# Performance work log

Hardware: AMD Instinct MI355X
Metric: run time of the kernel (lower is better)

## Reference

```python
import jax, jax.numpy as jnp
import numpy as np

N, E, B = 10000, 160000, 64
ND, ED, H, L, C = 128, 64, 256, 4, 10
LN_EPS = 1e-5


def _layernorm(x, g, b):
    mu = jnp.mean(x, axis=-1, keepdims=True)
    var = jnp.mean(jnp.square(x - mu), axis=-1, keepdims=True)
    return (x - mu) * jax.lax.rsqrt(var + LN_EPS) * g + b


def setup_inputs() -> dict:
    key = jax.random.key(0)
    ks = jax.random.split(key, 24)

    def w(k, shape, fan_in):
        return jax.random.normal(k, shape, jnp.float32) * (1.0 / np.sqrt(fan_in))

    node_features = jax.random.normal(ks[0], (N, ND), jnp.float32)
    edge_index = jax.random.randint(ks[1], (2, E), 0, N, jnp.int64)
    edge_features = jax.random.normal(ks[2], (E, ED), jnp.float32)
    # deterministic sorted batch assignment (no empty graphs)
    batch = (jnp.arange(N, dtype=jnp.int64) * B) // N

    inp = dict(
        node_features=node_features,
        edge_index=edge_index,
        edge_features=edge_features,
        batch=batch,
        node_W=w(ks[3], (ND, H), ND), node_b=jnp.zeros((H,), jnp.float32),
        edge_W=w(ks[4], (ED, H), ED), edge_b=jnp.zeros((H,), jnp.float32),
        msg_W1=w(ks[5], (L, 3 * H, H), 3 * H), msg_b1=jnp.zeros((L, H), jnp.float32),
        msg_W2=w(ks[6], (L, H, H), H), msg_b2=jnp.zeros((L, H), jnp.float32),
        upd_W1=w(ks[7], (L, 2 * H, H), 2 * H), upd_b1=jnp.zeros((L, H), jnp.float32),
        upd_W2=w(ks[8], (L, H, H), H), upd_b2=jnp.zeros((L, H), jnp.float32),
        ln_g=jnp.ones((L, H), jnp.float32), ln_b=jnp.zeros((L, H), jnp.float32),
        ro_W1=w(ks[9], (H, H), H), ro_b1=jnp.zeros((H,), jnp.float32),
        ro_W2=w(ks[10], (H, C), H), ro_b2=jnp.zeros((C,), jnp.float32),
    )
    return inp


def _forward(node_features, edge_features, node_W, node_b, edge_W, edge_b,
             msg_W1, msg_b1, msg_W2, msg_b2, upd_W1, upd_b1, upd_W2, upd_b2,
             ln_g, ln_b, ro_W1, ro_b1, ro_W2, ro_b2, edge_index, batch):
    src, dst = edge_index[0], edge_index[1]
    x = node_features @ node_W + node_b            # [N, H]
    edge_attr = edge_features @ edge_W + edge_b    # [E, H]
    for l in range(L):
        # batched gather-MLP over all edges (vectorized version of the per-edge loop)
        m_in = jnp.concatenate([x[src], x[dst], edge_attr], axis=-1)  # [E, 3H]
        msg = jax.nn.relu(m_in @ msg_W1[l] + msg_b1[l]) @ msg_W2[l] + msg_b2[l]
        agg = jnp.zeros_like(x).at[dst].add(msg)    # scatter-add by destination
        u_in = jnp.concatenate([x, agg], axis=-1)   # [N, 2H]
        upd = jax.nn.relu(u_in @ upd_W1[l] + upd_b1[l]) @ upd_W2[l] + upd_b2[l]
        x = _layernorm(x + upd, ln_g[l], ln_b[l])
    # global mean pool per graph
    sums = jax.ops.segment_sum(x, batch, num_segments=B)
    cnts = jax.ops.segment_sum(jnp.ones((x.shape[0], 1), x.dtype), batch, num_segments=B)
    pooled = sums / cnts                            # [B, H]
    return jax.nn.relu(pooled @ ro_W1 + ro_b1) @ ro_W2 + ro_b2  # [B, C]


def reference(node_features, edge_index, edge_features, batch,
              node_W, node_b, edge_W, edge_b,
              msg_W1, msg_b1, msg_W2, msg_b2,
              upd_W1, upd_b1, upd_W2, upd_b2,
              ln_g, ln_b, ro_W1, ro_b1, ro_W2, ro_b2):
    return _forward(node_features, edge_features, node_W, node_b, edge_W, edge_b,
                    msg_W1, msg_b1, msg_W2, msg_b2, upd_W1, upd_b1, upd_W2, upd_b2,
                    ln_g, ln_b, ro_W1, ro_b1, ro_W2, ro_b2, edge_index, batch)
```

## Files before the change

### kernel.cpp

```cpp
#include <hip/hip_runtime.h>
#include <cstdint>
#include <cstddef>


typedef unsigned short u16;
typedef __attribute__((ext_vector_type(4))) float f32x4;
typedef __attribute__((ext_vector_type(8))) short bf16x8;
typedef __attribute__((ext_vector_type(4))) short s16x4;

constexpr int kN  = 10000;
constexpr int kE  = 160000;
constexpr int kB  = 64;
constexpr int kH  = 256;
constexpr int kL  = 4;
constexpr int kC  = 10;
constexpr float kEps = 1e-5f;

struct __align__(16) F4 { float v[4]; };
__device__ __forceinline__ F4 ldF4(const float* p) { return *reinterpret_cast<const F4*>(p); }

__device__ __forceinline__ u16 f2bf(float f) {
    unsigned u = __builtin_bit_cast(unsigned, f);
    return (u16)((u + 0x7fffu + ((u >> 16) & 1u)) >> 16);
}
__device__ __forceinline__ float bf2f(u16 h) {
    return __builtin_bit_cast(float, (unsigned)h << 16);
}
__device__ __forceinline__ unsigned cvtpk(float lo, float hi) {
    unsigned r;
    asm("v_cvt_pk_bf16_f32 %0, %1, %2" : "=v"(r) : "v"(lo), "v"(hi));
    return r;
}

typedef __attribute__((address_space(1))) void GV;
typedef __attribute__((address_space(3))) void LV;
__device__ __forceinline__ void gl_lds16(const void* g, void* l) {
    __builtin_amdgcn_global_load_lds((GV*)g, (LV*)l, 16, 0, 0);
}
__device__ __forceinline__ void dma_w16k(const u16* __restrict__ Wc, char* lds, int tid) {
    const int w = tid >> 6, lane = tid & 63;
    char* lb = lds + w * 4096;
    const char* gb = (const char*)Wc + w * 4096 + lane * 16;
    #pragma unroll
    for (int i = 0; i < 4; ++i) gl_lds16(gb + i * 1024, lb + i * 1024);
}

__global__ void k_detect_i64(const unsigned* __restrict__ w, int* __restrict__ flag) {
    if (threadIdx.x == 0 && blockIdx.x == 0) {
        int is64 = 1;
        for (int i = 0; i < 64; ++i)
            if (w[2*i + 1] != 0u) { is64 = 0; break; }
        *flag = is64;
    }
}
__global__ void k_cvt_idx(const unsigned* __restrict__ w, const int* __restrict__ flag,
                          int* __restrict__ out, int n) {
    int i = blockIdx.x * 256 + threadIdx.x;
    if (i < n) out[i] = (*flag) ? (int)w[2*i] : (int)w[i];
}

__global__ __launch_bounds__(256) void k_hist(const int* __restrict__ dst,
                                              int* __restrict__ cnt) {
    int e = blockIdx.x * 256 + threadIdx.x;
    if (e < kE) atomicAdd(&cnt[dst[e]], 1);
}
__global__ __launch_bounds__(256) void k_scan(const int* __restrict__ cnt,
                                              int* __restrict__ cur) {
    __shared__ int part[256];
    const int t = threadIdx.x;
    const int per = (kN + 255) / 256;
    int s = 0;
    for (int i = 0; i < per; ++i) {
        int idx = t * per + i;
        if (idx < kN) s += cnt[idx];
    }
    int own = s;
    part[t] = s; __syncthreads();
    for (int off = 1; off < 256; off <<= 1) {
        int v = (t >= off) ? part[t - off] : 0;
        __syncthreads();
        part[t] += v;
        __syncthreads();
    }
    int run = part[t] - own;
    for (int i = 0; i < per; ++i) {
        int idx = t * per + i;
        if (idx < kN) { cur[idx] = run; run += cnt[idx]; }
    }
}
__global__ __launch_bounds__(256) void k_scatter(
    const int* __restrict__ src, const int* __restrict__ dst,
    int* __restrict__ cur, int* __restrict__ perm,
    int* __restrict__ ssorted, int* __restrict__ dsorted) {
    int e = blockIdx.x * 256 + threadIdx.x;
    if (e < kE) {
        int d = dst[e];
        int p = atomicAdd(&cur[d], 1);
        perm[p] = e;
        ssorted[p] = src[e];
        dsorted[p] = d;
    }
}

__global__ __launch_bounds__(256) void k_prep_w(
    const float* __restrict__ mW1, const float* __restrict__ mW2,
    const float* __restrict__ uW1, const float* __restrict__ uW2,
    u16* __restrict__ tm1, u16* __restrict__ tm2,
    u16* __restrict__ tu1, u16* __restrict__ tu2)
{
    int idx = blockIdx.x * 256 + threadIdx.x;
    const int S1 = kL * 768 * 256;
    const int S2 = S1 + kL * 256 * 256;
    const int S3 = S2 + kL * 512 * 256;
    const int S4 = S3 + kL * 256 * 256;
    const float* src; u16* dst; int K, r;
    if (idx < S1)      { src = mW1; dst = tm1; K = 768; r = idx; }
    else if (idx < S2) { src = mW2; dst = tm2; K = 256; r = idx - S1; }
    else if (idx < S3) { src = uW1; dst = tu1; K = 512; r = idx - S2; }
    else if (idx < S4) { src = uW2; dst = tu2; K = 256; r = idx - S3; }
    else return;
    int per = K * 256;
    int layer = r / per, rr = r - layer * per;
    int k = rr >> 8, n = rr & 255;
    int kc = k >> 5, kg = (k >> 3) & 3, e = k & 7;
    dst[(size_t)layer * per + (size_t)kc * 8192 + n * 32 + ((kg ^ ((n >> 1) & 3)) << 3) + e]
        = f2bf(src[(size_t)layer * per + rr]);
}

__global__ __launch_bounds__(256) void k_prep_ef(
    const float* __restrict__ ef, const int* __restrict__ perm,
    u16* __restrict__ efs)
{
    int idx = blockIdx.x * 256 + threadIdx.x;
    if (idx >= kE * 64) return;
    int p = idx >> 6, k = idx & 63;
    float v = ef[(size_t)perm[p] * 64 + k];
    int row = p & 63, blk = p >> 6;
    int kc = k >> 5, kg = (k >> 3) & 3, e = k & 7;
    efs[(size_t)blk * 4096 + kc * 2048 + row * 32
        + ((kg ^ ((row >> 1) & 3)) << 3) + e] = f2bf(v);
}

__global__ __launch_bounds__(256) void k_prep_m(
    const float* __restrict__ eW, const float* __restrict__ eb,
    const float* __restrict__ mW1, const float* __restrict__ mb1,
    u16* __restrict__ tmc, float* __restrict__ b1p)
{
    __shared__ float sWe[16 * 256];
    const int l = blockIdx.x, rq = blockIdx.y, t = threadIdx.x;
    const int r0 = rq * 16;
    #pragma unroll
    for (int i = 0; i < 16; ++i) sWe[i * 256 + t] = eW[(size_t)(r0 + i) * 256 + t];
    __syncthreads();
    const float* W1c = mW1 + (size_t)l * 768 * 256 + (size_t)512 * 256;
    float m[16];
    #pragma unroll
    for (int r = 0; r < 16; ++r) m[r] = 0.f;
    float bp = (rq == 0) ? mb1[l * 256 + t] : 0.f;
    for (int j = 0; j < 256; ++j) {
        float wv = W1c[(size_t)j * 256 + t];
        if (rq == 0) bp = fmaf(eb[j], wv, bp);
        #pragma unroll
        for (int r = 0; r < 16; ++r) m[r] = fmaf(sWe[r * 256 + j], wv, m[r]);
    }
    if (rq == 0) b1p[l * 256 + t] = bp;
    #pragma unroll
    for (int r = 0; r < 16; ++r) {
        int k = r0 + r;
        int kc = k >> 5, kg = (k >> 3) & 3, e = k & 7;
        tmc[(size_t)l * 16384 + (size_t)kc * 8192 + t * 32
            + ((kg ^ ((t >> 1) & 3)) << 3) + e] = f2bf(m[r]);
    }
}

__global__ __launch_bounds__(256) void k_encode_nodes(
    const float* __restrict__ nf, const float* __restrict__ W,
    const float* __restrict__ b, float* __restrict__ x, u16* __restrict__ x_bf)
{
    __shared__ float s_nf[4 * 128];
    const int n0 = blockIdx.x * 4;
    const int tid = threadIdx.x;
    reinterpret_cast<float2*>(s_nf)[tid] =
        reinterpret_cast<const float2*>(nf + (size_t)n0 * 128)[tid];
    __syncthreads();
    float acc[4] = {0.f, 0.f, 0.f, 0.f};
    for (int k = 0; k < 128; ++k) {
        float w = W[k * kH + tid];
        #pragma unroll
        for (int r = 0; r < 4; ++r) acc[r] = fmaf(s_nf[r * 128 + k], w, acc[r]);
    }
    float bias = b[tid];
    #pragma unroll
    for (int r = 0; r < 4; ++r) {
        float o = acc[r] + bias;
        x[(size_t)(n0 + r) * kH + tid] = o;
        x_bf[(size_t)(n0 + r) * kH + tid] = f2bf(o);
    }
}

__device__ __forceinline__ bf16x8 rdfrag(const char* lds, int n, int kg) {
    return *reinterpret_cast<const bf16x8*>(lds + n * 64 + ((kg ^ ((n >> 1) & 3)) << 4));
}
__device__ __forceinline__ bf16x8 rdH(const char* H, int row, int kbyte) {
    return *reinterpret_cast<const bf16x8*>(H + row * 512 + (kbyte ^ ((row & 7) << 4)));
}

__global__ __launch_bounds__(256, 3) void k_node_pre(
    const u16* __restrict__ x_bf, const u16* __restrict__ Wt1,
    u16* __restrict__ y_a, u16* __restrict__ y_b)
{
    __shared__ char sWt[16384];
    __shared__ char sA[4096];
    const int tid = threadIdx.x;
    const int n0 = blockIdx.x * 64;
    const int half = blockIdx.y;
    const u16* Wt = Wt1 + (size_t)half * 8 * 8192;
    u16* y = half ? y_b : y_a;
    const int w = tid >> 6, lane = tid & 63;
    const int lr = lane & 15, lg = lane >> 4;
    const int srow = tid >> 2, skg = tid & 3;
    const int kg_src = skg ^ ((srow >> 1) & 3);
    int gnode = n0 + srow; if (gnode >= kN) gnode = kN - 1;

    f32x4 acc[4][4];
    #pragma unroll
    for (int i = 0; i < 4; ++i)
        #pragma unroll
        for (int j = 0; j < 4; ++j) acc[i][j] = (f32x4){0.f, 0.f, 0.f, 0.f};

    for (int kc = 0; kc < 8; ++kc) {
        __syncthreads();
        dma_w16k(Wt + (size_t)kc * 8192, sWt, tid);
        gl_lds16(x_bf + (size_t)gnode * kH + kc * 32 + kg_src * 8, sA + w * 1024);
        __syncthreads();
        bf16x8 af[4], bfm[4];
        #pragma unroll
        for (int i = 0; i < 4; ++i) af[i] = rdfrag(sWt, w * 64 + i * 16 + lr, lg);
        #pragma unroll
        for (int j = 0; j < 4; ++j) bfm[j] = rdfrag(sA, j * 16 + lr, lg);
        #pragma unroll
        for (int i = 0; i < 4; ++i)
            #pragma unroll
            for (int j = 0; j < 4; ++j)
                acc[i][j] = __builtin_amdgcn_mfma_f32_16x16x32_bf16(af[i], bfm[j], acc[i][j], 0, 0, 0);
    }
    #pragma unroll
    for (int i = 0; i < 4; ++i) {
        const int hc0 = w * 64 + i * 16 + lg * 4;
        #pragma unroll
        for (int j = 0; j < 4; ++j) {
            const int node = n0 + j * 16 + lr;
            if (node < kN) {
                uint2 o;
                o.x = cvtpk(acc[i][j][0], acc[i][j][1]);
                o.y = cvtpk(acc[i][j][2], acc[i][j][3]);
                *reinterpret_cast<uint2*>(y + (size_t)node * kH + hc0) = o;
            }
        }
    }
}

__global__ __launch_bounds__(256, 3) void k_msg(
    const u16* __restrict__ efs,
    const int* __restrict__ ssorted, const int* __restrict__ dsorted,
    const u16* __restrict__ y_a, const u16* __restrict__ y_b,
    const u16* __restrict__ Wtm, const float* __restrict__ b1p,
    const u16* __restrict__ Wt2, const float* __restrict__ b2,
    float* __restrict__ agg)
{
    __shared__ char sWt[16384];
    __shared__ char sA[4096];
    __shared__ char sH[32768];
    __shared__ int sDst[64];

    const int tid = threadIdx.x;
    const int nwg = gridDim.x;
    const int q8 = nwg >> 3, r8 = nwg & 7;
    const int xcd = blockIdx.x & 7, sub = blockIdx.x >> 3;
    const int bid = (xcd < r8 ? xcd * (q8 + 1) : r8 * (q8 + 1) + (xcd - r8) * q8) + sub;
    const int e0 = bid * 64;

    const int w = tid >> 6, lane = tid & 63;
    const int lr = lane & 15, lg = lane >> 4;

    if (tid < 64) sDst[tid] = dsorted[e0 + tid];
    int esrc[4], edst[4];
    #pragma unroll
    for (int j = 0; j < 4; ++j) {
        esrc[j] = ssorted[e0 + j * 16 + lr];
        edst[j] = dsorted[e0 + j * 16 + lr];
    }

    f32x4 acc[4][4];
    #pragma unroll
    for (int i = 0; i < 4; ++i)
        #pragma unroll
        for (int j = 0; j < 4; ++j) acc[i][j] = (f32x4){0.f, 0.f, 0.f, 0.f};

    for (int kc = 0; kc < 2; ++kc) {
        __syncthreads();
        dma_w16k(Wtm + (size_t)kc * 8192, sWt, tid);
        gl_lds16((const char*)efs + (size_t)bid * 8192 + kc * 4096 + w * 1024 + lane * 16,
                 sA + w * 1024);
        __syncthreads();
        bf16x8 af[4], bfm[4];
        #pragma unroll
        for (int i = 0; i < 4; ++i) af[i] = rdfrag(sWt, w * 64 + i * 16 + lr, lg);
        #pragma unroll
        for (int j = 0; j < 4; ++j) bfm[j] = rdfrag(sA, j * 16 + lr, lg);
        #pragma unroll
        for (int i = 0; i < 4; ++i)
            #pragma unroll
            for (int j = 0; j < 4; ++j)
                acc[i][j] = __builtin_amdgcn_mfma_f32_16x16x32_bf16(af[i], bfm[j], acc[i][j], 0, 0, 0);
    }

    #pragma unroll
    for (int j = 0; j < 4; ++j) {
        const int edge = j * 16 + lr;
        const u16* pa = y_a + (size_t)esrc[j] * kH;
        const u16* pb = y_b + (size_t)edst[j] * kH;
        uint2 ya[4], yb[4];
        #pragma unroll
        for (int i = 0; i < 4; ++i) {
            const int hc0 = w * 64 + i * 16 + lg * 4;
            ya[i] = *reinterpret_cast<const uint2*>(pa + hc0);
            yb[i] = *reinterpret_cast<const uint2*>(pb + hc0);
        }
        #pragma unroll
        for (int i = 0; i < 4; ++i) {
            const int hc0 = w * 64 + i * 16 + lg * 4;
            const F4 bb = ldF4(b1p + hc0);
            float s0 = __builtin_bit_cast(float, ya[i].x << 16) + __builtin_bit_cast(float, yb[i].x << 16);
            float s1 = __builtin_bit_cast(float, ya[i].x & 0xffff0000u) + __builtin_bit_cast(float, yb[i].x & 0xffff0000u);
            float s2 = __builtin_bit_cast(float, ya[i].y << 16) + __builtin_bit_cast(float, yb[i].y << 16);
            float s3 = __builtin_bit_cast(float, ya[i].y & 0xffff0000u) + __builtin_bit_cast(float, yb[i].y & 0xffff0000u);
            float h0 = acc[i][j][0] + bb.v[0] + s0; h0 = h0 > 0.f ? h0 : 0.f;
            float h1 = acc[i][j][1] + bb.v[1] + s1; h1 = h1 > 0.f ? h1 : 0.f;
            float h2 = acc[i][j][2] + bb.v[2] + s2; h2 = h2 > 0.f ? h2 : 0.f;
            float h3 = acc[i][j][3] + bb.v[3] + s3; h3 = h3 > 0.f ? h3 : 0.f;
            uint2 o; o.x = cvtpk(h0, h1); o.y = cvtpk(h2, h3);
            int byte = edge * 512 + hc0 * 2;
            *reinterpret_cast<uint2*>(sH + (byte ^ ((edge & 7) << 4))) = o;
            acc[i][j] = (f32x4){0.f, 0.f, 0.f, 0.f};
        }
    }
    __syncthreads();

    for (int kc = 0; kc < 8; ++kc) {
        __syncthreads();
        dma_w16k(Wt2 + (size_t)kc * 8192, sWt, tid);
        __syncthreads();
        bf16x8 af2[4], bf2[4];
        #pragma unroll
        for (int i = 0; i < 4; ++i) af2[i] = rdH(sH, i * 16 + lr, kc * 64 + lg * 16);
        #pragma unroll
        for (int j = 0; j < 4; ++j) bf2[j] = rdfrag(sWt, w * 64 + j * 16 + lr, lg);
        #pragma unroll
        for (int i = 0; i < 4; ++i)
            #pragma unroll
            for (int j = 0; j < 4; ++j)
                acc[i][j] = __builtin_amdgcn_mfma_f32_16x16x32_bf16(af2[i], bf2[j], acc[i][j], 0, 0, 0);
    }

    __syncthreads();
    #pragma unroll
    for (int j = 0; j < 4; ++j) {
        const int oc = w * 64 + j * 16 + lr;
        const float b2v = b2[oc];
        #pragma unroll
        for (int i = 0; i < 4; ++i) {
            unsigned p01 = cvtpk(acc[i][j][0] + b2v, acc[i][j][1] + b2v);
            unsigned p23 = cvtpk(acc[i][j][2] + b2v, acc[i][j][3] + b2v);
            int eb0 = i * 16 + lg * 4;
            *reinterpret_cast<u16*>(sH + (((eb0 + 0) * 512 + oc * 2) ^ (((eb0 + 0) & 7) << 4))) = (u16)p01;
            *reinterpret_cast<u16*>(sH + (((eb0 + 1) * 512 + oc * 2) ^ (((eb0 + 1) & 7) << 4))) = (u16)(p01 >> 16);
            *reinterpret_cast<u16*>(sH + (((eb0 + 2) * 512 + oc * 2) ^ (((eb0 + 2) & 7) << 4))) = (u16)p23;
            *reinterpret_cast<u16*>(sH + (((eb0 + 3) * 512 + oc * 2) ^ (((eb0 + 3) & 7) << 4))) = (u16)(p23 >> 16);
        }
    }
    __syncthreads();

    {
        const int col = tid;
        float run = 0.f;
        int prev = sDst[0];
        #pragma unroll 1
        for (int eb = 0; eb < 8; ++eb) {
            float vv[8]; int dd[8];
            #pragma unroll
            for (int t = 0; t < 8; ++t) {
                int e = eb * 8 + t;
                int byte = e * 512 + col * 2;
                vv[t] = bf2f(*reinterpret_cast<const u16*>(sH + (byte ^ ((e & 7) << 4))));
                dd[t] = sDst[e];
            }
            #pragma unroll
            for (int t = 0; t < 8; ++t) {
                if (dd[t] != prev) {
                    unsafeAtomicAdd(agg + (size_t)prev * kH + col, run);
                    run = 0.f; prev = dd[t];
                }
                run += vv[t];
            }
        }
        unsafeAtomicAdd(agg + (size_t)prev * kH + col, run);
    }
}

__global__ __launch_bounds__(256, 2) void k_upd(
    float* __restrict__ x, u16* __restrict__ x_bf,
    float* __restrict__ agg,
    const u16* __restrict__ Wt1, const float* __restrict__ b1,
    const u16* __restrict__ Wt2, const float* __restrict__ b2,
    const float* __restrict__ lng, const float* __restrict__ lnb,
    const u16* __restrict__ Wt1n, int do_y,
    u16* __restrict__ y_a, u16* __restrict__ y_b)
{
    __shared__ char sWt[2][16384];
    __shared__ char sA[2][4096];
    __shared__ char sH[32768];

    const int tid = threadIdx.x;
    const int n0 = blockIdx.x * 64;
    const int w = tid >> 6, lane = tid & 63;
    const int lr = lane & 15, lg = lane >> 4;
    const int srow = tid >> 2, skg = tid & 3;
    const int kg_src = skg ^ ((srow >> 1) & 3);
    int gnode = n0 + srow; if (gnode >= kN) gnode = kN - 1;

    dma_w16k(Wt1, sWt[0], tid);
    gl_lds16(x_bf + (size_t)gnode * kH + kg_src * 8, sA[0] + w * 1024);

    f32x4 acc[4][4];
    #pragma unroll
    for (int i = 0; i < 4; ++i)
        #pragma unroll
        for (int j = 0; j < 4; ++j) acc[i][j] = (f32x4){0.f, 0.f, 0.f, 0.f};
    __syncthreads();

    for (int kc = 0; kc < 16; ++kc) {
        const int cur = kc & 1, nxt = cur ^ 1;
        bool do_agg = false; F4 a0, a1;
        if (kc < 15) {
            dma_w16k(Wt1 + (size_t)(kc + 1) * 8192, sWt[nxt], tid);
            if (kc + 1 < 8) {
                gl_lds16(x_bf + (size_t)gnode * kH + (kc + 1) * 32 + kg_src * 8,
                         sA[nxt] + w * 1024);
            } else {
                const float* ap = agg + (size_t)gnode * kH + (kc + 1 - 8) * 32 + skg * 8;
                a0 = ldF4(ap); a1 = ldF4(ap + 4); do_agg = true;
            }
        } else {
            dma_w16k(Wt2, sWt[nxt], tid);
        }
        bf16x8 af[4], bfm[4];
        #pragma unroll
        for (int i = 0; i < 4; ++i) af[i] = rdfrag(sWt[cur], w * 64 + i * 16 + lr, lg);
        #pragma unroll
        for (int j = 0; j < 4; ++j) bfm[j] = rdfrag(sA[cur], j * 16 + lr, lg);
        #pragma unroll
        for (int i = 0; i < 4; ++i)
            #pragma unroll
            for (int j = 0; j < 4; ++j)
                acc[i][j] = __builtin_amdgcn_mfma_f32_16x16x32_bf16(af[i], bfm[j], acc[i][j], 0, 0, 0);
        if (do_agg) {
            int4 bv;
            bv.x = (int)cvtpk(a0.v[0], a0.v[1]);
            bv.y = (int)cvtpk(a0.v[2], a0.v[3]);
            bv.z = (int)cvtpk(a1.v[0], a1.v[1]);
            bv.w = (int)cvtpk(a1.v[2], a1.v[3]);
            *reinterpret_cast<int4*>(sA[nxt] + srow * 64 + ((skg ^ ((srow >> 1) & 3)) << 4)) = bv;
        }
        __syncthreads();
    }

    #pragma unroll
    for (int i = 0; i < 4; ++i) {
        const int hc0 = w * 64 + i * 16 + lg * 4;
        const F4 bb = ldF4(b1 + hc0);
        #pragma unroll
        for (int j = 0; j < 4; ++j) {
            const int row = j * 16 + lr;
            float h0 = acc[i][j][0] + bb.v[0]; h0 = h0 > 0.f ? h0 : 0.f;
            float h1 = acc[i][j][1] + bb.v[1]; h1 = h1 > 0.f ? h1 : 0.f;
            float h2 = acc[i][j][2] + bb.v[2]; h2 = h2 > 0.f ? h2 : 0.f;
            float h3 = acc[i][j][3] + bb.v[3]; h3 = h3 > 0.f ? h3 : 0.f;
            uint2 o; o.x = cvtpk(h0, h1); o.y = cvtpk(h2, h3);
            int byte = row * 512 + hc0 * 2;
            *reinterpret_cast<uint2*>(sH + (byte ^ ((row & 7) << 4))) = o;
            acc[i][j] = (f32x4){0.f, 0.f, 0.f, 0.f};
        }
    }
    __syncthreads();

    {
        float4 z = make_float4(0.f, 0.f, 0.f, 0.f);
        float4* bp = reinterpret_cast<float4*>(agg + (size_t)n0 * kH);
        #pragma unroll
        for (int i = 0; i < 16; ++i) {
            int idx = i * 256 + tid;
            int row = idx >> 6;
            if (n0 + row < kN) bp[idx] = z;
        }
    }

    for (int kc = 0; kc < 8; ++kc) {
        const int cur = kc & 1, nxt = cur ^ 1;
        if (kc < 7) dma_w16k(Wt2 + (size_t)(kc + 1) * 8192, sWt[nxt], tid);
        bf16x8 af2[4], bf2[4];
        #pragma unroll
        for (int i = 0; i < 4; ++i) af2[i] = rdH(sH, i * 16 + lr, kc * 64 + lg * 16);
        #pragma unroll
        for (int j = 0; j < 4; ++j) bf2[j] = rdfrag(sWt[cur], w * 64 + j * 16 + lr, lg);
        #pragma unroll
        for (int i = 0; i < 4; ++i)
            #pragma unroll
            for (int j = 0; j < 4; ++j)
                acc[i][j] = __builtin_amdgcn_mfma_f32_16x16x32_bf16(af2[i], bf2[j], acc[i][j], 0, 0, 0);
        __syncthreads();
    }

    float b2v[4], gv[4], bvn[4];
    #pragma unroll
    for (int j = 0; j < 4; ++j) {
        int oc = w * 64 + j * 16 + lr;
        b2v[j] = b2[oc]; gv[j] = lng[oc]; bvn[j] = lnb[oc];
    }
    #pragma unroll
    for (int i = 0; i < 4; ++i)
        #pragma unroll
        for (int j = 0; j < 4; ++j) {
            int oc = w * 64 + j * 16 + lr;
            #pragma unroll
            for (int q = 0; q < 4; ++q) {
                int node = n0 + i * 16 + lg * 4 + q;
                int ncl = node < kN ? node : kN - 1;
                acc[i][j][q] += b2v[j] + x[(size_t)ncl * kH + oc];
            }
        }

    float (*red)[64][2] = reinterpret_cast<float(*)[64][2]>(sA[0]);
    float2* mstd = reinterpret_cast<float2*>(sA[0] + 2048);
    __syncthreads();
    #pragma unroll
    for (int i = 0; i < 4; ++i)
        #pragma unroll
        for (int q = 0; q < 4; ++q) {
            float s = acc[i][0][q] + acc[i][1][q] + acc[i][2][q] + acc[i][3][q];
            float ss = acc[i][0][q] * acc[i][0][q] + acc[i][1][q] * acc[i][1][q]
                     + acc[i][2][q] * acc[i][2][q] + acc[i][3][q] * acc[i][3][q];
            #pragma unroll
            for (int m = 1; m < 16; m <<= 1) { s += __shfl_xor(s, m); ss += __shfl_xor(ss, m); }
            if (lr == 0) { red[w][i * 16 + lg * 4 + q][0] = s; red[w][i * 16 + lg * 4 + q][1] = ss; }
        }
    __syncthreads();
    if (tid < 64) {
        float s = red[0][tid][0] + red[1][tid][0] + red[2][tid][0] + red[3][tid][0];
        float ss = red[0][tid][1] + red[1][tid][1] + red[2][tid][1] + red[3][tid][1];
        float mean = s * (1.f / 256.f);
        float var = ss * (1.f / 256.f) - mean * mean;
        mstd[tid] = make_float2(mean, rsqrtf(var + kEps));
    }
    __syncthreads();
    #pragma unroll
    for (int i = 0; i < 4; ++i)
        #pragma unroll
        for (int j = 0; j < 4; ++j) {
            int oc = w * 64 + j * 16 + lr;
            #pragma unroll
            for (int q = 0; q < 4; ++q) {
                int nn = i * 16 + lg * 4 + q;
                int node = n0 + nn;
                if (node < kN) {
                    float2 ms = mstd[nn];
                    float o = (acc[i][j][q] - ms.x) * ms.y * gv[j] + bvn[j];
                    u16 ob = f2bf(o);
                    x[(size_t)node * kH + oc] = o;
                    x_bf[(size_t)node * kH + oc] = ob;
                    if (do_y) {
                        int byte = nn * 512 + oc * 2;
                        *reinterpret_cast<u16*>(sH + (byte ^ ((nn & 7) << 4))) = ob;
                    }
                }
            }
        }

    if (do_y) {
        __syncthreads();
        dma_w16k(Wt1n, sWt[0], tid);
        #pragma unroll
        for (int i = 0; i < 4; ++i)
            #pragma unroll
            for (int j = 0; j < 4; ++j) acc[i][j] = (f32x4){0.f, 0.f, 0.f, 0.f};
        __syncthreads();
        for (int c = 0; c < 16; ++c) {
            const int cur = c & 1;
            if (c < 15) dma_w16k(Wt1n + (size_t)(c + 1) * 8192, sWt[cur ^ 1], tid);
            bf16x8 af[4], bfm[4];
            #pragma unroll
            for (int i = 0; i < 4; ++i) af[i] = rdfrag(sWt[cur], w * 64 + i * 16 + lr, lg);
            #pragma unroll
            for (int j = 0; j < 4; ++j) bfm[j] = rdH(sH, j * 16 + lr, (c & 7) * 64 + lg * 16);
            #pragma unroll
            for (int i = 0; i < 4; ++i)
                #pragma unroll
                for (int j = 0; j < 4; ++j)
                    acc[i][j] = __builtin_amdgcn_mfma_f32_16x16x32_bf16(af[i], bfm[j], acc[i][j], 0, 0, 0);
            if (c == 7 || c == 15) {
                u16* y = (c == 7) ? y_a : y_b;
                #pragma unroll
                for (int i = 0; i < 4; ++i) {
                    const int hc0 = w * 64 + i * 16 + lg * 4;
                    #pragma unroll
                    for (int j = 0; j < 4; ++j) {
                        const int node = n0 + j * 16 + lr;
                        if (node < kN) {
                            uint2 o;
                            o.x = cvtpk(acc[i][j][0], acc[i][j][1]);
                            o.y = cvtpk(acc[i][j][2], acc[i][j][3]);
                            *reinterpret_cast<uint2*>(y + (size_t)node * kH + hc0) = o;
                        }
                        acc[i][j] = (f32x4){0.f, 0.f, 0.f, 0.f};
                    }
                }
            }
            __syncthreads();
        }
    }
}

__device__ __forceinline__ int lower_bound_i(const int* a, int n, int v) {
    int lo = 0, hi = n;
    while (lo < hi) { int m = (lo + hi) >> 1; if (a[m] < v) lo = m + 1; else hi = m; }
    return lo;
}

__global__ __launch_bounds__(256) void k_pool_ro(
    const float* __restrict__ x, const int* __restrict__ batch,
    const float* __restrict__ W1, const float* __restrict__ b1,
    const float* __restrict__ W2, const float* __restrict__ b2,
    float* __restrict__ out)
{
    __shared__ float ph[kH];
    __shared__ float h1[kH];
    const int b = blockIdx.x, t = threadIdx.x;
    const int s = lower_bound_i(batch, kN, b);
    const int e = lower_bound_i(batch, kN, b + 1);
    float acc = 0.f;
    for (int i = s; i < e; ++i) acc += x[(size_t)i * kH + t];
    ph[t] = acc / (float)(e - s);
    __syncthreads();
    float a = b1[t];
    for (int k = 0; k < kH; ++k) a = fmaf(ph[k], W1[k * kH + t], a);
    h1[t] = a > 0.f ? a : 0.f;
    __syncthreads();
    if (t < kC) {
        float o = b2[t];
        for (int k = 0; k < kH; ++k) o = fmaf(h1[k], W2[k * kC + t], o);
        out[b * kC + t] = o;
    }
}

extern "C" void kernel_launch(void* const* d_in, const int* in_sizes, int n_in,
                              void* d_out, int out_size, void* d_ws, size_t ws_size,
                              hipStream_t stream)
{
    const float* nf     = (const float*)d_in[0];
    const void*  ei_raw = d_in[1];
    const float* ef     = (const float*)d_in[2];
    const void*  ba_raw = d_in[3];
    const float* node_W = (const float*)d_in[4];
    const float* node_b = (const float*)d_in[5];
    const float* edge_W = (const float*)d_in[6];
    const float* edge_b = (const float*)d_in[7];
    const float* msg_W1 = (const float*)d_in[8];
    const float* msg_b1 = (const float*)d_in[9];
    const float* msg_W2 = (const float*)d_in[10];
    const float* msg_b2 = (const float*)d_in[11];
    const float* upd_W1 = (const float*)d_in[12];
    const float* upd_b1 = (const float*)d_in[13];
    const float* upd_W2 = (const float*)d_in[14];
    const float* upd_b2 = (const float*)d_in[15];
    const float* ln_g   = (const float*)d_in[16];
    const float* ln_b   = (const float*)d_in[17];
    const float* ro_W1  = (const float*)d_in[18];
    const float* ro_b1  = (const float*)d_in[19];
    const float* ro_W2  = (const float*)d_in[20];
    const float* ro_b2  = (const float*)d_in[21];

    char* p = (char*)d_ws;
    auto alloc = [&](size_t bytes) { char* r = p; p += (bytes + 255) & ~(size_t)255; return r; };
    float* x    = (float*)alloc((size_t)kN * kH * 4);
    float* agg  = (float*)alloc((size_t)kN * kH * 4);
    u16* x_bf   = (u16*)alloc((size_t)kN * kH * 2);
    u16* y_a    = (u16*)alloc((size_t)kN * kH * 2);
    u16* y_b    = (u16*)alloc((size_t)kN * kH * 2);
    u16* efs    = (u16*)alloc((size_t)kE * 64 * 2);
    u16* tm1 = (u16*)alloc((size_t)kL * 768 * 256 * 2);
    u16* tm2 = (u16*)alloc((size_t)kL * 256 * 256 * 2);
    u16* tu1 = (u16*)alloc((size_t)kL * 512 * 256 * 2);
    u16* tu2 = (u16*)alloc((size_t)kL * 256 * 256 * 2);
    u16* tmc = (u16*)alloc((size_t)kL * 64 * 256 * 2);
    float* b1p = (float*)alloc((size_t)kL * 256 * 4);
    int* ei32 = (int*)alloc((size_t)2 * kE * 4);
    int* ba32 = (int*)alloc((size_t)kN * 4);
    int* cnt  = (int*)alloc((size_t)kN * 4);
    int* cur  = (int*)alloc((size_t)kN * 4);
    int* perm = (int*)alloc((size_t)kE * 4);
    int* ssorted = (int*)alloc((size_t)kE * 4);
    int* dsorted = (int*)alloc((size_t)kE * 4);
    int* flag = (int*)alloc(4);

    k_detect_i64<<<1, 64, 0, stream>>>((const unsigned*)ei_raw, flag);
    k_cvt_idx<<<(2 * kE + 255) / 256, 256, 0, stream>>>((const unsigned*)ei_raw, flag, ei32, 2 * kE);
    k_cvt_idx<<<(kN + 255) / 256, 256, 0, stream>>>((const unsigned*)ba_raw, flag, ba32, kN);
    const int* src = ei32;
    const int* dst = ei32 + kE;

    hipMemsetAsync(cnt, 0, (size_t)kN * 4, stream);
    k_hist<<<(kE + 255) / 256, 256, 0, stream>>>(dst, cnt);
    k_scan<<<1, 256, 0, stream>>>(cnt, cur);
    k_scatter<<<(kE + 255) / 256, 256, 0, stream>>>(src, dst, cur, perm, ssorted, dsorted);

    const int prep_elems = kL * (768 + 256 + 512 + 256) * 256;
    k_prep_w<<<(prep_elems + 255) / 256, 256, 0, stream>>>(
        msg_W1, msg_W2, upd_W1, upd_W2, tm1, tm2, tu1, tu2);
    k_prep_m<<<dim3(kL, 4), 256, 0, stream>>>(edge_W, edge_b, msg_W1, msg_b1, tmc, b1p);
    k_prep_ef<<<(kE * 64 + 255) / 256, 256, 0, stream>>>(ef, perm, efs);

    k_encode_nodes<<<kN / 4, 256, 0, stream>>>(nf, node_W, node_b, x, x_bf);

    hipMemsetAsync(agg, 0, (size_t)kN * kH * sizeof(float), stream);
    k_node_pre<<<dim3((kN + 63) / 64, 2), 256, 0, stream>>>(x_bf, tm1, y_a, y_b);

    for (int l = 0; l < kL; ++l) {
        k_msg<<<kE / 64, 256, 0, stream>>>(efs, ssorted, dsorted, y_a, y_b,
            tmc + (size_t)l * 64 * 256, b1p + l * 256,
            tm2 + (size_t)l * 256 * 256, msg_b2 + l * kH, agg);
        const int do_y = (l < kL - 1) ? 1 : 0;
        k_upd<<<(kN + 63) / 64, 256, 0, stream>>>(x, x_bf, agg,
            tu1 + (size_t)l * 512 * 256, upd_b1 + l * kH,
            tu2 + (size_t)l * 256 * 256, upd_b2 + l * kH,
            ln_g + l * kH, ln_b + l * kH,
            tm1 + (size_t)(l + 1 < kL ? l + 1 : 0) * 768 * 256, do_y, y_a, y_b);
    }

    k_pool_ro<<<kB, 256, 0, stream>>>(x, ba32, ro_W1, ro_b1, ro_W2, ro_b2, (float*)d_out);
}
```

Measured before the change: 658.6 us.

## Read msg weights from global directly, split node projection out of update kernel

k_msg no longer stages weight and edge-feature tiles in LDS with barriers. It reads MFMA fragments straight from global memory, prefetches the gathered y rows up front and raises the occupancy hint to 4. The next-layer node projection that was fused into k_upd moves back to a separate k_node_pre launch per layer, which adds an extra pass over x_bf per layer but simplifies k_upd. k_prep_ef now reads edge features coalesced and scatters writes via a rank array instead of gathering through perm. The risk is uncached, uncoalesced weight-fragment reads in k_msg and more register pressure from the prefetched y values.

After: 607.0 us. -7.8%, faster.

```diff
diff --git a/kernel.cpp b/kernel.cpp
--- a/kernel.cpp
+++ b/kernel.cpp
@@ -43,6 +43,16 @@
     const char* gb = (const char*)Wc + w * 4096 + lane * 16;
     #pragma unroll
     for (int i = 0; i < 4; ++i) gl_lds16(gb + i * 1024, lb + i * 1024);
+}
+
+__device__ __forceinline__ bf16x8 g_frag(const u16* __restrict__ g, int n, int kg) {
+    return *reinterpret_cast<const bf16x8*>(g + n * 32 + ((kg ^ ((n >> 1) & 3)) << 3));
+}
+__device__ __forceinline__ bf16x8 rdfrag(const char* lds, int n, int kg) {
+    return *reinterpret_cast<const bf16x8*>(lds + n * 64 + ((kg ^ ((n >> 1) & 3)) << 4));
+}
+__device__ __forceinline__ bf16x8 rdH(const char* H, int row, int kbyte) {
+    return *reinterpret_cast<const bf16x8*>(H + row * 512 + (kbyte ^ ((row & 7) << 4)));
 }
 
 __global__ void k_detect_i64(const unsigned* __restrict__ w, int* __restrict__ flag) {
@@ -90,13 +100,13 @@
 }
 __global__ __launch_bounds__(256) void k_scatter(
     const int* __restrict__ src, const int* __restrict__ dst,
-    int* __restrict__ cur, int* __restrict__ perm,
+    int* __restrict__ cur, int* __restrict__ rank,
     int* __restrict__ ssorted, int* __restrict__ dsorted) {
     int e = blockIdx.x * 256 + threadIdx.x;
     if (e < kE) {
         int d = dst[e];
         int p = atomicAdd(&cur[d], 1);
-        perm[p] = e;
+        rank[e] = p;
         ssorted[p] = src[e];
         dsorted[p] = d;
     }
@@ -128,17 +138,18 @@
 }
 
 __global__ __launch_bounds__(256) void k_prep_ef(
-    const float* __restrict__ ef, const int* __restrict__ perm,
+    const float* __restrict__ ef, const int* __restrict__ rank,
     u16* __restrict__ efs)
 {
     int idx = blockIdx.x * 256 + threadIdx.x;
     if (idx >= kE * 64) return;
-    int p = idx >> 6, k = idx & 63;
-    float v = ef[(size_t)perm[p] * 64 + k];
+    int e = idx >> 6, k = idx & 63;
+    float v = ef[idx];
+    int p = rank[e];
     int row = p & 63, blk = p >> 6;
-    int kc = k >> 5, kg = (k >> 3) & 3, e = k & 7;
+    int kc = k >> 5, kg = (k >> 3) & 3, ee = k & 7;
     efs[(size_t)blk * 4096 + kc * 2048 + row * 32
-        + ((kg ^ ((row >> 1) & 3)) << 3) + e] = f2bf(v);
+        + ((kg ^ ((row >> 1) & 3)) << 3) + ee] = f2bf(v);
 }
 
 __global__ __launch_bounds__(256) void k_prep_m(
@@ -196,13 +207,6 @@
         x[(size_t)(n0 + r) * kH + tid] = o;
         x_bf[(size_t)(n0 + r) * kH + tid] = f2bf(o);
     }
-}
-
-__device__ __forceinline__ bf16x8 rdfrag(const char* lds, int n, int kg) {
-    return *reinterpret_cast<const bf16x8*>(lds + n * 64 + ((kg ^ ((n >> 1) & 3)) << 4));
-}
-__device__ __forceinline__ bf16x8 rdH(const char* H, int row, int kbyte) {
-    return *reinterpret_cast<const bf16x8*>(H + row * 512 + (kbyte ^ ((row & 7) << 4)));
 }
 
 __global__ __launch_bounds__(256, 3) void k_node_pre(
@@ -260,7 +264,7 @@
     }
 }
 
-__global__ __launch_bounds__(256, 3) void k_msg(
+__global__ __launch_bounds__(256, 4) void k_msg(
     const u16* __restrict__ efs,
     const int* __restrict__ ssorted, const int* __restrict__ dsorted,
     const u16* __restrict__ y_a, const u16* __restrict__ y_b,
@@ -268,8 +272,6 @@
     const u16* __restrict__ Wt2, const float* __restrict__ b2,
     float* __restrict__ agg)
 {
-    __shared__ char sWt[16384];
-    __shared__ char sA[4096];
     __shared__ char sH[32768];
     __shared__ int sDst[64];
 
@@ -284,11 +286,20 @@
     const int lr = lane & 15, lg = lane >> 4;
 
     if (tid < 64) sDst[tid] = dsorted[e0 + tid];
-    int esrc[4], edst[4];
+
+    uint2 ya[4][4], yb[4][4];
     #pragma unroll
     for (int j = 0; j < 4; ++j) {
-        esrc[j] = ssorted[e0 + j * 16 + lr];
-        edst[j] = dsorted[e0 + j * 16 + lr];
+        const int es = ssorted[e0 + j * 16 + lr];
+        const int ed = dsorted[e0 + j * 16 + lr];
+        const u16* pa = y_a + (size_t)es * kH;
+        const u16* pb = y_b + (size_t)ed * kH;
+        #pragma unroll
+        for (int i = 0; i < 4; ++i) {
+            const int hc0 = w * 64 + i * 16 + lg * 4;
+            ya[j][i] = *reinterpret_cast<const uint2*>(pa + hc0);
+            yb[j][i] = *reinterpret_cast<const uint2*>(pb + hc0);
+        }
     }
 
     f32x4 acc[4][4];
@@ -297,17 +308,18 @@
         #pragma unroll
         for (int j = 0; j < 4; ++j) acc[i][j] = (f32x4){0.f, 0.f, 0.f, 0.f};
 
+    #pragma unroll
     for (int kc = 0; kc < 2; ++kc) {
-        __syncthreads();
-        dma_w16k(Wtm + (size_t)kc * 8192, sWt, tid);
-        gl_lds16((const char*)efs + (size_t)bid * 8192 + kc * 4096 + w * 1024 + lane * 16,
-                 sA + w * 1024);
-        __syncthreads();
+        const u16* efc = efs + (size_t)bid * 4096 + kc * 2048;
         bf16x8 af[4], bfm[4];
         #pragma unroll
-        for (int i = 0; i < 4; ++i) af[i] = rdfrag(sWt, w * 64 + i * 16 + lr, lg);
-        #pragma unroll
-        for (int j = 0; j < 4; ++j) bfm[j] = rdfrag(sA, j * 16 + lr, lg);
+        for (int i = 0; i < 4; ++i) af[i] = g_frag(Wtm + kc * 8192, w * 64 + i * 16 + lr, lg);
+        #pragma unroll
+        for (int j = 0; j < 4; ++j) {
+            int row = j * 16 + lr;
+            bfm[j] = *reinterpret_cast<const bf16x8*>(
+                efc + row * 32 + ((lg ^ ((row >> 1) & 3)) << 3));
+        }
         #pragma unroll
         for (int i = 0; i < 4; ++i)
             #pragma unroll
@@ -318,23 +330,14 @@
     #pragma unroll
     for (int j = 0; j < 4; ++j) {
         const int edge = j * 16 + lr;
-        const u16* pa = y_a + (size_t)esrc[j] * kH;
-        const u16* pb = y_b + (size_t)edst[j] * kH;
-        uint2 ya[4], yb[4];
-        #pragma unroll
-        for (int i = 0; i < 4; ++i) {
-            const int hc0 = w * 64 + i * 16 + lg * 4;
-            ya[i] = *reinterpret_cast<const uint2*>(pa + hc0);
-            yb[i] = *reinterpret_cast<const uint2*>(pb + hc0);
-        }
         #pragma unroll
         for (int i = 0; i < 4; ++i) {
             const int hc0 = w * 64 + i * 16 + lg * 4;
             const F4 bb = ldF4(b1p + hc0);
-            float s0 = __builtin_bit_cast(float, ya[i].x << 16) + __builtin_bit_cast(float, yb[i].x << 16);
-            float s1 = __builtin_bit_cast(float, ya[i].x & 0xffff0000u) + __builtin_bit_cast(float, yb[i].x & 0xffff0000u);
-            float s2 = __builtin_bit_cast(float, ya[i].y << 16) + __builtin_bit_cast(float, yb[i].y << 16);
-            float s3 = __builtin_bit_cast(float, ya[i].y & 0xffff0000u) + __builtin_bit_cast(float, yb[i].y & 0xffff0000u);
+            float s0 = __builtin_bit_cast(float, ya[j][i].x << 16) + __builtin_bit_cast(float, yb[j][i].x << 16);
+            float s1 = __builtin_bit_cast(float, ya[j][i].x & 0xffff0000u) + __builtin_bit_cast(float, yb[j][i].x & 0xffff0000u);
+            float s2 = __builtin_bit_cast(float, ya[j][i].y << 16) + __builtin_bit_cast(float, yb[j][i].y << 16);
+            float s3 = __builtin_bit_cast(float, ya[j][i].y & 0xffff0000u) + __builtin_bit_cast(float, yb[j][i].y & 0xffff0000u);
             float h0 = acc[i][j][0] + bb.v[0] + s0; h0 = h0 > 0.f ? h0 : 0.f;
             float h1 = acc[i][j][1] + bb.v[1] + s1; h1 = h1 > 0.f ? h1 : 0.f;
             float h2 = acc[i][j][2] + bb.v[2] + s2; h2 = h2 > 0.f ? h2 : 0.f;
@@ -347,15 +350,13 @@
     }
     __syncthreads();
 
+    #pragma unroll 2
     for (int kc = 0; kc < 8; ++kc) {
-        __syncthreads();
-        dma_w16k(Wt2 + (size_t)kc * 8192, sWt, tid);
-        __syncthreads();
         bf16x8 af2[4], bf2[4];
         #pragma unroll
         for (int i = 0; i < 4; ++i) af2[i] = rdH(sH, i * 16 + lr, kc * 64 + lg * 16);
         #pragma unroll
-        for (int j = 0; j < 4; ++j) bf2[j] = rdfrag(sWt, w * 64 + j * 16 + lr, lg);
+        for (int j = 0; j < 4; ++j) bf2[j] = g_frag(Wt2 + kc * 8192, w * 64 + j * 16 + lr, lg);
         #pragma unroll
         for (int i = 0; i < 4; ++i)
             #pragma unroll
@@ -413,9 +414,7 @@
     float* __restrict__ agg,
     const u16* __restrict__ Wt1, const float* __restrict__ b1,
     const u16* __restrict__ Wt2, const float* __restrict__ b2,
-    const float* __restrict__ lng, const float* __restrict__ lnb,
-    const u16* __restrict__ Wt1n, int do_y,
-    u16* __restrict__ y_a, u16* __restrict__ y_b)
+    const float* __restrict__ lng, const float* __restrict__ lnb)
 {
     __shared__ char sWt[2][16384];
     __shared__ char sA[2][4096];
@@ -575,59 +574,11 @@
                 if (node < kN) {
                     float2 ms = mstd[nn];
                     float o = (acc[i][j][q] - ms.x) * ms.y * gv[j] + bvn[j];
-                    u16 ob = f2bf(o);
                     x[(size_t)node * kH + oc] = o;
-                    x_bf[(size_t)node * kH + oc] = ob;
-                    if (do_y) {
-                        int byte = nn * 512 + oc * 2;
-                        *reinterpret_cast<u16*>(sH + (byte ^ ((nn & 7) << 4))) = ob;
-                    }
+                    x_bf[(size_t)node * kH + oc] = f2bf(o);
                 }
             }
         }
-
-    if (do_y) {
-        __syncthreads();
-        dma_w16k(Wt1n, sWt[0], tid);
-        #pragma unroll
-        for (int i = 0; i < 4; ++i)
-            #pragma unroll
-            for (int j = 0; j < 4; ++j) acc[i][j] = (f32x4){0.f, 0.f, 0.f, 0.f};
-        __syncthreads();
-        for (int c = 0; c < 16; ++c) {
-            const int cur = c & 1;
-            if (c < 15) dma_w16k(Wt1n + (size_t)(c + 1) * 8192, sWt[cur ^ 1], tid);
-            bf16x8 af[4], bfm[4];
-            #pragma unroll
-            for (int i = 0; i < 4; ++i) af[i] = rdfrag(sWt[cur], w * 64 + i * 16 + lr, lg);
-            #pragma unroll
-            for (int j = 0; j < 4; ++j) bfm[j] = rdH(sH, j * 16 + lr, (c & 7) * 64 + lg * 16);
-            #pragma unroll
-            for (int i = 0; i < 4; ++i)
-                #pragma unroll
-                for (int j = 0; j < 4; ++j)
-                    acc[i][j] = __builtin_amdgcn_mfma_f32_16x16x32_bf16(af[i], bfm[j], acc[i][j], 0, 0, 0);
-            if (c == 7 || c == 15) {
-                u16* y = (c == 7) ? y_a : y_b;
-                #pragma unroll
-                for (int i = 0; i < 4; ++i) {
-                    const int hc0 = w * 64 + i * 16 + lg * 4;
-                    #pragma unroll
-                    for (int j = 0; j < 4; ++j) {
-                        const int node = n0 + j * 16 + lr;
-                        if (node < kN) {
-                            uint2 o;
-                            o.x = cvtpk(acc[i][j][0], acc[i][j][1]);
-                            o.y = cvtpk(acc[i][j][2], acc[i][j][3]);
-                            *reinterpret_cast<uint2*>(y + (size_t)node * kH + hc0) = o;
-                        }
-                        acc[i][j] = (f32x4){0.f, 0.f, 0.f, 0.f};
-                    }
-                }
-            }
-            __syncthreads();
-        }
-    }
 }
 
 __device__ __forceinline__ int lower_bound_i(const int* a, int n, int v) {
@@ -707,7 +658,7 @@
     int* ba32 = (int*)alloc((size_t)kN * 4);
     int* cnt  = (int*)alloc((size_t)kN * 4);
     int* cur  = (int*)alloc((size_t)kN * 4);
-    int* perm = (int*)alloc((size_t)kE * 4);
+    int* rank = (int*)alloc((size_t)kE * 4);
     int* ssorted = (int*)alloc((size_t)kE * 4);
     int* dsorted = (int*)alloc((size_t)kE * 4);
     int* flag = (int*)alloc(4);
@@ -721,29 +672,27 @@
     hipMemsetAsync(cnt, 0, (size_t)kN * 4, stream);
     k_hist<<<(kE + 255) / 256, 256, 0, stream>>>(dst, cnt);
     k_scan<<<1, 256, 0, stream>>>(cnt, cur);
-    k_scatter<<<(kE + 255) / 256, 256, 0, stream>>>(src, dst, cur, perm, ssorted, dsorted);
+    k_scatter<<<(kE + 255) / 256, 256, 0, stream>>>(src, dst, cur, rank, ssorted, dsorted);
 
     const int prep_elems = kL * (768 + 256 + 512 + 256) * 256;
     k_prep_w<<<(prep_elems + 255) / 256, 256, 0, stream>>>(
         msg_W1, msg_W2, upd_W1, upd_W2, tm1, tm2, tu1, tu2);
     k_prep_m<<<dim3(kL, 4), 256, 0, stream>>>(edge_W, edge_b, msg_W1, msg_b1, tmc, b1p);
-    k_prep_ef<<<(kE * 64 + 255) / 256, 256, 0, stream>>>(ef, perm, efs);
+    k_prep_ef<<<(kE * 64 + 255) / 256, 256, 0, stream>>>(ef, rank, efs);
 
     k_encode_nodes<<<kN / 4, 256, 0, stream>>>(nf, node_W, node_b, x, x_bf);
-
     hipMemsetAsync(agg, 0, (size_t)kN * kH * sizeof(float), stream);
-    k_node_pre<<<dim3((kN + 63) / 64, 2), 256, 0, stream>>>(x_bf, tm1, y_a, y_b);
 
     for (int l = 0; l < kL; ++l) {
+        k_node_pre<<<dim3((kN + 63) / 64, 2), 256, 0, stream>>>(
+            x_bf, tm1 + (size_t)l * 768 * 256, y_a, y_b);
         k_msg<<<kE / 64, 256, 0, stream>>>(efs, ssorted, dsorted, y_a, y_b,
             tmc + (size_t)l * 64 * 256, b1p + l * 256,
             tm2 + (size_t)l * 256 * 256, msg_b2 + l * kH, agg);
-        const int do_y = (l < kL - 1) ? 1 : 0;
         k_upd<<<(kN + 63) / 64, 256, 0, stream>>>(x, x_bf, agg,
             tu1 + (size_t)l * 512 * 256, upd_b1 + l * kH,
             tu2 + (size_t)l * 256 * 256, upd_b2 + l * kH,
-            ln_g + l * kH, ln_b + l * kH,
-            tm1 + (size_t)(l + 1 < kL ? l + 1 : 0) * 768 * 256, do_y, y_a, y_b);
+            ln_g + l * kH, ln_b + l * kH);
     }
 
     k_pool_ro<<<kB, 256, 0, stream>>>(x, ba32, ro_W1, ro_b1, ro_W2, ro_b2, (float*)d_out);
```
